# Kernel optimization log

Measured on AMD Instinct MI355X. Metric: run time of the kernel, lower is better.

Reference implementation:

```python
import jax, jax.numpy as jnp
import numpy as np

B, T, C, H, D = 2048, 64, 64, 8, 64  # batch, block_size, n_embed, num_heads, head_size


def setup_inputs() -> dict:
    key = jax.random.key(0)
    ks = jax.random.split(key, 6)
    s = C ** -0.5  # approx torch Linear init scale
    x = jax.random.normal(ks[0], (B, T, C), dtype=jnp.float32)
    Wq = jax.random.uniform(ks[1], (H, C, D), jnp.float32, -s, s)  # per-head query weights (in, out)
    Wk = jax.random.uniform(ks[2], (H, C, D), jnp.float32, -s, s)
    Wv = jax.random.uniform(ks[3], (H, C, D), jnp.float32, -s, s)
    sp = (H * D) ** -0.5
    Wproj = jax.random.uniform(ks[4], (H * D, C), jnp.float32, -sp, sp)  # proj weight (in, out)
    bproj = jax.random.uniform(ks[5], (C,), jnp.float32, -sp, sp)
    return {"x": x, "Wq": Wq, "Wk": Wk, "Wv": Wv, "Wproj": Wproj, "bproj": bproj}


def reference(x, Wq, Wk, Wv, Wproj, bproj):
    # per-head projections, vectorized over heads (original loops over Head modules)
    q = jnp.einsum('btc,hcd->bhtd', x, Wq)
    k = jnp.einsum('btc,hcd->bhtd', x, Wk)
    v = jnp.einsum('btc,hcd->bhtd', x, Wv)
    scores = jnp.einsum('bhtd,bhsd->bhts', q, k) * (D ** -0.5)  # [B,H,T,T]
    causal = jnp.tril(jnp.ones((T, T), dtype=bool))
    scores = jnp.where(causal, scores, jnp.float32(-jnp.inf))
    wei = jax.nn.softmax(scores, axis=-1)  # dropout = identity in eval mode
    out = jnp.einsum('bhts,bhsd->bhtd', wei, v)
    out = out.transpose(0, 2, 1, 3).reshape(B, T, H * D)  # concat heads on last dim
    out = out @ Wproj + bproj  # output projection (dropout = identity in eval)
    return out
```

## Files before the change

### kernel.cpp

```cpp
#include <hip/hip_runtime.h>

typedef __bf16 bf16x8 __attribute__((ext_vector_type(8)));
typedef float f32x4 __attribute__((ext_vector_type(4)));
typedef unsigned short u16x4 __attribute__((ext_vector_type(4)));
typedef unsigned short u16x8 __attribute__((ext_vector_type(8)));
typedef unsigned int u32x4 __attribute__((ext_vector_type(4)));

#define LDA 72

template <int N> struct Int { static constexpr int value = N; };

__device__ __forceinline__ unsigned short f2bf(float f) {
  __bf16 b = (__bf16)f;
  return __builtin_bit_cast(unsigned short, b);
}

__device__ __forceinline__ u16x4 pack4(f32x4 v) {
  u16x4 r;
  r[0] = f2bf(v[0]); r[1] = f2bf(v[1]); r[2] = f2bf(v[2]); r[3] = f2bf(v[3]);
  return r;
}

__device__ __forceinline__ bf16x8 frag8(const unsigned short* p) {
  return __builtin_bit_cast(bf16x8, *reinterpret_cast<const u16x8*>(p));
}

#define MFMA(a, b, c) __builtin_amdgcn_mfma_f32_16x16x32_bf16(a, b, c, 0, 0, 0)

__device__ __forceinline__ void cfrag2bfrag(const f32x4 v[4], bf16x8 out[2]) {
  unsigned O[4][2];
  #pragma unroll
  for (int si = 0; si < 4; ++si) {
    u16x4 p = pack4(v[si]);
    O[si][0] = (unsigned)p[0] | ((unsigned)p[1] << 16);
    O[si][1] = (unsigned)p[2] | ((unsigned)p[3] << 16);
  }
  unsigned H[2][2][2];
  #pragma unroll
  for (int s1 = 0; s1 < 2; ++s1)
    #pragma unroll
    for (int d = 0; d < 2; ++d) {
      auto r = __builtin_amdgcn_permlane32_swap(O[2 * s1][d], O[2 * s1 + 1][d], false, false);
      H[s1][0][d] = r[0];
      H[s1][1][d] = r[1];
    }
  #pragma unroll
  for (int e1 = 0; e1 < 2; ++e1) {
    auto r0 = __builtin_amdgcn_permlane16_swap(H[e1][0][0], H[e1][1][0], false, false);
    auto r1 = __builtin_amdgcn_permlane16_swap(H[e1][0][1], H[e1][1][1], false, false);
    u32x4 f;
    f[0] = r0[0]; f[1] = r1[0]; f[2] = r0[1]; f[3] = r1[1];
    out[e1] = __builtin_bit_cast(bf16x8, f);
  }
}

__global__ __launch_bounds__(256) void fuse_pack(
    const float* __restrict__ Wq, const float* __restrict__ Wk,
    const float* __restrict__ Wv, const float* __restrict__ Wp,
    unsigned short* __restrict__ wf) {
  __shared__ float A[64 * 65];
  __shared__ float B[64 * 65];
  const int blk = blockIdx.x;
  const int t = blk >> 3, h = blk & 7;
  const int tid = threadIdx.x;
  const float* Asrc = (t ? Wv : Wq) + h * 4096;
  const float* Bsrc = (t ? Wp : Wk) + h * 4096;
  for (int i = tid; i < 4096; i += 256) {
    A[(i >> 6) * 65 + (i & 63)] = Asrc[i];
    B[(i >> 6) * 65 + (i & 63)] = Bsrc[i];
  }
  __syncthreads();
  unsigned short* dst = wf + blk * 4096;
  for (int o = 0; o < 16; ++o) {
    int idx = o * 256 + tid;
    int k = idx >> 6, n = idx & 63;
    float s = 0.f;
    if (t == 0) {
      for (int d = 0; d < 64; ++d) s += A[k * 65 + d] * B[n * 65 + d];
      s *= 0.18033688f;
    } else {
      for (int d = 0; d < 64; ++d) s += A[k * 65 + d] * B[d * 65 + n];
    }
    int kk = k >> 5, i = k & 7, lg = (k >> 3) & 3, si = n >> 4, l15 = n & 15;
    dst[((kk * 4 + si) * 64 + lg * 16 + l15) * 8 + i] = f2bf(s);
  }
}

__global__ __launch_bounds__(256, 4) void mha_fwd(
    const float* __restrict__ x, const unsigned short* __restrict__ wf,
    const float* __restrict__ bproj, float* __restrict__ out) {
  __shared__ __attribute__((aligned(16))) unsigned char smem[32768];
  unsigned short* XsBase = reinterpret_cast<unsigned short*>(smem);
  unsigned short* ZsBase = reinterpret_cast<unsigned short*>(smem);

  const int tid  = threadIdx.x;
  const int lane = tid & 63;
  const int w    = tid >> 6;
  const int bt   = w >> 1;
  const int mg   = w & 1;
  const int l15  = lane & 15;
  const int g    = lane >> 4;
  const int kcol = 8 * g;

  const float* xb = x + (size_t)blockIdx.x * 8192;
  #pragma unroll
  for (int it = 0; it < 8; ++it) {
    int idx = it * 1024 + tid * 4;
    float4 v = *reinterpret_cast<const float4*>(xb + idx);
    f32x4 vv = {v.x, v.y, v.z, v.w};
    int sb = idx >> 12, rem = idx & 4095;
    *reinterpret_cast<u16x4*>(&XsBase[sb * (64 * LDA) + (rem >> 6) * LDA + (rem & 63)]) = pack4(vv);
  }
  __syncthreads();

  bf16x8 xf[2][4];
  #pragma unroll
  for (int cc = 0; cc < 2; ++cc)
    #pragma unroll
    for (int t = 0; t < 4; ++t)
      xf[cc][t] = frag8(&XsBase[bt * (64 * LDA) + (t * 16 + l15) * LDA + cc * 32 + kcol]);
  __syncthreads();

  f32x4 oacc[2][4];
  #pragma unroll
  for (int nt = 0; nt < 4; ++nt) {
    float bias = bproj[nt * 16 + l15];
    f32x4 bv = {bias, bias, bias, bias};
    oacc[0][nt] = bv;
    oacc[1][nt] = bv;
  }

  #pragma unroll 1
  for (int h = 0; h < 8; ++h) {
    const unsigned short* mf = wf + h * 4096;
    const unsigned short* nf = wf + 32768 + h * 4096;
    unsigned short* zs = ZsBase + ((bt * 2 + (h & 1)) * 8) * 64 * 8;

    auto head_body = [&](auto MT0C, auto MT1C) {
      constexpr int MT0 = decltype(MT0C)::value;
      constexpr int MT1 = decltype(MT1C)::value;

      #pragma unroll
      for (int l = 0; l < 2; ++l) {
        const int ntg = 2 * mg + l;
        bf16x8 nf0 = frag8(&nf[ntg * 512 + lane * 8]);
        bf16x8 nf1 = frag8(&nf[(4 + ntg) * 512 + lane * 8]);
        f32x4 zc[4] = {};
        #pragma unroll
        for (int st = 0; st < 4; ++st) {
          zc[st] = MFMA(xf[0][st], nf0, zc[st]);
          zc[st] = MFMA(xf[1][st], nf1, zc[st]);
        }
        bf16x8 zb[2];
        cfrag2bfrag(zc, zb);
        #pragma unroll
        for (int cc = 0; cc < 2; ++cc)
          *reinterpret_cast<u16x8*>(&zs[((ntg * 2 + cc) * 64 + lane) * 8]) =
              __builtin_bit_cast(u16x8, zb[cc]);
      }

      bf16x8 pA[2][2];
      auto gs = [&](auto MTC, int lmt) {
        constexpr int MT = decltype(MTC)::value;
        f32x4 gc[4] = {};
        #pragma unroll
        for (int kk = 0; kk < 2; ++kk)
          #pragma unroll
          for (int ct = 0; ct < 4; ++ct)
            gc[ct] = MFMA(frag8(&mf[(kk * 4 + ct) * 512 + lane * 8]), xf[kk][MT], gc[ct]);
        bf16x8 gB[2];
        cfrag2bfrag(gc, gB);

        f32x4 sc[4] = {};
        #pragma unroll
        for (int cc = 0; cc < 2; ++cc)
          #pragma unroll
          for (int st = 0; st < 4; ++st)
            if (st <= MT)
              sc[st] = MFMA(xf[cc][st], gB[cc], sc[st]);

        const int m = MT * 16 + l15;
        float sum = 0.f;
        #pragma unroll
        for (int st = 0; st < 4; ++st) {
          if (st < MT) {
            #pragma unroll
            for (int r = 0; r < 4; ++r) { float e = exp2f(sc[st][r]); sc[st][r] = e; sum += e; }
          } else if (st == MT) {
            #pragma unroll
            for (int r = 0; r < 4; ++r) {
              int s = st * 16 + 4 * g + r;
              float e = (s <= m) ? exp2f(sc[st][r]) : 0.f;
              sc[st][r] = e; sum += e;
            }
          }
        }
        sum += __shfl_xor(sum, 16);
        sum += __shfl_xor(sum, 32);
        float rinv = __builtin_amdgcn_rcpf(sum);
        #pragma unroll
        for (int st = 0; st < 4; ++st)
          if (st <= MT) sc[st] *= rinv;
        bf16x8 o2[2];
        cfrag2bfrag(sc, o2);
        pA[0][lmt] = o2[0]; pA[1][lmt] = o2[1];
      };
      gs(Int<MT0>{}, 0);
      gs(Int<MT1>{}, 1);

      __syncthreads();

      #pragma unroll
      for (int nt = 0; nt < 4; ++nt) {
        bf16x8 zb0 = frag8(&zs[((nt * 2 + 0) * 64 + lane) * 8]);
        oacc[0][nt] = MFMA(pA[0][0], zb0, oacc[0][nt]);
        oacc[1][nt] = MFMA(pA[0][1], zb0, oacc[1][nt]);
        bf16x8 zb1 = frag8(&zs[((nt * 2 + 1) * 64 + lane) * 8]);
        if (MT0 >= 2) oacc[0][nt] = MFMA(pA[1][0], zb1, oacc[0][nt]);
        if (MT1 >= 2) oacc[1][nt] = MFMA(pA[1][1], zb1, oacc[1][nt]);
      }
    };

    if (mg == 0) head_body(Int<0>{}, Int<3>{});
    else         head_body(Int<1>{}, Int<2>{});
  }

  const int mtv0 = mg ? 1 : 0;
  const int mtv1 = mg ? 2 : 3;
  float* ob = out + ((size_t)blockIdx.x * 2 + bt) * 4096;
  #pragma unroll
  for (int lmt = 0; lmt < 2; ++lmt) {
    int mt = lmt ? mtv1 : mtv0;
    #pragma unroll
    for (int r = 0; r < 4; ++r) {
      float* orow = ob + (mt * 16 + 4 * g + r) * 64;
      #pragma unroll
      for (int nt = 0; nt < 4; ++nt)
        orow[nt * 16 + l15] = oacc[lmt][nt][r];
    }
  }
}

extern "C" void kernel_launch(void* const* d_in, const int* in_sizes, int n_in,
                              void* d_out, int out_size, void* d_ws, size_t ws_size,
                              hipStream_t stream) {
  const float* x  = (const float*)d_in[0];
  const float* Wq = (const float*)d_in[1];
  const float* Wk = (const float*)d_in[2];
  const float* Wv = (const float*)d_in[3];
  const float* Wp = (const float*)d_in[4];
  const float* bp = (const float*)d_in[5];
  unsigned short* wf = (unsigned short*)d_ws;

  fuse_pack<<<dim3(16), dim3(256), 0, stream>>>(Wq, Wk, Wv, Wp, wf);
  mha_fwd<<<dim3(1024), dim3(256), 0, stream>>>(x, wf, bp, (float*)d_out);
}
```

Measured before the change: 58.52 us.

## Process one batch per block with one query tile per wave

Each workgroup now handles a single batch element instead of two. Each of the four waves owns one 16-row query tile, replacing the paired balanced tiles (0+3, 1+2). Shared memory halves and the grid doubles, which may raise occupancy and lower register pressure. The cost is causal load imbalance across waves at each per-head barrier.

After: 61.33 us. 4.8% more time.

```diff
diff --git a/kernel.cpp b/kernel.cpp
--- a/kernel.cpp
+++ b/kernel.cpp
@@ -89,27 +89,24 @@
 __global__ __launch_bounds__(256, 4) void mha_fwd(
     const float* __restrict__ x, const unsigned short* __restrict__ wf,
     const float* __restrict__ bproj, float* __restrict__ out) {
-  __shared__ __attribute__((aligned(16))) unsigned char smem[32768];
+  __shared__ __attribute__((aligned(16))) unsigned char smem[16384];
   unsigned short* XsBase = reinterpret_cast<unsigned short*>(smem);
   unsigned short* ZsBase = reinterpret_cast<unsigned short*>(smem);
 
   const int tid  = threadIdx.x;
   const int lane = tid & 63;
   const int w    = tid >> 6;
-  const int bt   = w >> 1;
-  const int mg   = w & 1;
   const int l15  = lane & 15;
   const int g    = lane >> 4;
   const int kcol = 8 * g;
 
-  const float* xb = x + (size_t)blockIdx.x * 8192;
-  #pragma unroll
-  for (int it = 0; it < 8; ++it) {
+  const float* xb = x + (size_t)blockIdx.x * 4096;
+  #pragma unroll
+  for (int it = 0; it < 4; ++it) {
     int idx = it * 1024 + tid * 4;
     float4 v = *reinterpret_cast<const float4*>(xb + idx);
     f32x4 vv = {v.x, v.y, v.z, v.w};
-    int sb = idx >> 12, rem = idx & 4095;
-    *reinterpret_cast<u16x4*>(&XsBase[sb * (64 * LDA) + (rem >> 6) * LDA + (rem & 63)]) = pack4(vv);
+    *reinterpret_cast<u16x4*>(&XsBase[(idx >> 6) * LDA + (idx & 63)]) = pack4(vv);
   }
   __syncthreads();
 
@@ -118,33 +115,28 @@
   for (int cc = 0; cc < 2; ++cc)
     #pragma unroll
     for (int t = 0; t < 4; ++t)
-      xf[cc][t] = frag8(&XsBase[bt * (64 * LDA) + (t * 16 + l15) * LDA + cc * 32 + kcol]);
+      xf[cc][t] = frag8(&XsBase[(t * 16 + l15) * LDA + cc * 32 + kcol]);
   __syncthreads();
 
-  f32x4 oacc[2][4];
+  f32x4 oacc[4];
   #pragma unroll
   for (int nt = 0; nt < 4; ++nt) {
     float bias = bproj[nt * 16 + l15];
-    f32x4 bv = {bias, bias, bias, bias};
-    oacc[0][nt] = bv;
-    oacc[1][nt] = bv;
+    oacc[nt] = f32x4{bias, bias, bias, bias};
   }
 
   #pragma unroll 1
   for (int h = 0; h < 8; ++h) {
     const unsigned short* mf = wf + h * 4096;
     const unsigned short* nf = wf + 32768 + h * 4096;
-    unsigned short* zs = ZsBase + ((bt * 2 + (h & 1)) * 8) * 64 * 8;
-
-    auto head_body = [&](auto MT0C, auto MT1C) {
-      constexpr int MT0 = decltype(MT0C)::value;
-      constexpr int MT1 = decltype(MT1C)::value;
-
-      #pragma unroll
-      for (int l = 0; l < 2; ++l) {
-        const int ntg = 2 * mg + l;
-        bf16x8 nf0 = frag8(&nf[ntg * 512 + lane * 8]);
-        bf16x8 nf1 = frag8(&nf[(4 + ntg) * 512 + lane * 8]);
+    unsigned short* zs = ZsBase + (h & 1) * 4096;
+
+    auto head_body = [&](auto MTC) {
+      constexpr int MT = decltype(MTC)::value;
+
+      {
+        bf16x8 nf0 = frag8(&nf[MT * 512 + lane * 8]);
+        bf16x8 nf1 = frag8(&nf[(4 + MT) * 512 + lane * 8]);
         f32x4 zc[4] = {};
         #pragma unroll
         for (int st = 0; st < 4; ++st) {
@@ -155,22 +147,23 @@
         cfrag2bfrag(zc, zb);
         #pragma unroll
         for (int cc = 0; cc < 2; ++cc)
-          *reinterpret_cast<u16x8*>(&zs[((ntg * 2 + cc) * 64 + lane) * 8]) =
+          *reinterpret_cast<u16x8*>(&zs[((MT * 2 + cc) * 64 + lane) * 8]) =
               __builtin_bit_cast(u16x8, zb[cc]);
       }
 
-      bf16x8 pA[2][2];
-      auto gs = [&](auto MTC, int lmt) {
-        constexpr int MT = decltype(MTC)::value;
+      bf16x8 gB[2];
+      {
         f32x4 gc[4] = {};
         #pragma unroll
         for (int kk = 0; kk < 2; ++kk)
           #pragma unroll
           for (int ct = 0; ct < 4; ++ct)
             gc[ct] = MFMA(frag8(&mf[(kk * 4 + ct) * 512 + lane * 8]), xf[kk][MT], gc[ct]);
-        bf16x8 gB[2];
         cfrag2bfrag(gc, gB);
-
+      }
+
+      bf16x8 pA[2];
+      {
         f32x4 sc[4] = {};
         #pragma unroll
         for (int cc = 0; cc < 2; ++cc)
@@ -201,43 +194,35 @@
         #pragma unroll
         for (int st = 0; st < 4; ++st)
           if (st <= MT) sc[st] *= rinv;
-        bf16x8 o2[2];
-        cfrag2bfrag(sc, o2);
-        pA[0][lmt] = o2[0]; pA[1][lmt] = o2[1];
-      };
-      gs(Int<MT0>{}, 0);
-      gs(Int<MT1>{}, 1);
+        cfrag2bfrag(sc, pA);
+      }
 
       __syncthreads();
 
       #pragma unroll
       for (int nt = 0; nt < 4; ++nt) {
         bf16x8 zb0 = frag8(&zs[((nt * 2 + 0) * 64 + lane) * 8]);
-        oacc[0][nt] = MFMA(pA[0][0], zb0, oacc[0][nt]);
-        oacc[1][nt] = MFMA(pA[0][1], zb0, oacc[1][nt]);
-        bf16x8 zb1 = frag8(&zs[((nt * 2 + 1) * 64 + lane) * 8]);
-        if (MT0 >= 2) oacc[0][nt] = MFMA(pA[1][0], zb1, oacc[0][nt]);
-        if (MT1 >= 2) oacc[1][nt] = MFMA(pA[1][1], zb1, oacc[1][nt]);
+        oacc[nt] = MFMA(pA[0], zb0, oacc[nt]);
+        if (MT >= 2) {
+          bf16x8 zb1 = frag8(&zs[((nt * 2 + 1) * 64 + lane) * 8]);
+          oacc[nt] = MFMA(pA[1], zb1, oacc[nt]);
+        }
       }
     };
 
-    if (mg == 0) head_body(Int<0>{}, Int<3>{});
-    else         head_body(Int<1>{}, Int<2>{});
-  }
-
-  const int mtv0 = mg ? 1 : 0;
-  const int mtv1 = mg ? 2 : 3;
-  float* ob = out + ((size_t)blockIdx.x * 2 + bt) * 4096;
-  #pragma unroll
-  for (int lmt = 0; lmt < 2; ++lmt) {
-    int mt = lmt ? mtv1 : mtv0;
+    if      (w == 0) head_body(Int<0>{});
+    else if (w == 1) head_body(Int<1>{});
+    else if (w == 2) head_body(Int<2>{});
+    else             head_body(Int<3>{});
+  }
+
+  float* ob = out + (size_t)blockIdx.x * 4096;
+  #pragma unroll
+  for (int r = 0; r < 4; ++r) {
+    float* orow = ob + (w * 16 + 4 * g + r) * 64;
     #pragma unroll
-    for (int r = 0; r < 4; ++r) {
-      float* orow = ob + (mt * 16 + 4 * g + r) * 64;
-      #pragma unroll
-      for (int nt = 0; nt < 4; ++nt)
-        orow[nt * 16 + l15] = oacc[lmt][nt][r];
-    }
+    for (int nt = 0; nt < 4; ++nt)
+      orow[nt * 16 + l15] = oacc[nt][r];
   }
 }
 
@@ -253,5 +238,5 @@
   unsigned short* wf = (unsigned short*)d_ws;
 
   fuse_pack<<<dim3(16), dim3(256), 0, stream>>>(Wq, Wk, Wv, Wp, wf);
-  mha_fwd<<<dim3(1024), dim3(256), 0, stream>>>(x, wf, bp, (float*)d_out);
-}
+  mha_fwd<<<dim3(2048), dim3(256), 0, stream>>>(x, wf, bp, (float*)d_out);
+}
```
